# Kernel optimization log

Hardware: AMD Instinct MI355X
Metric: run time of the kernel (lower is better)

## Reference

```python
import jax, jax.numpy as jnp
import numpy as np

D_IN = 1024
D_OUT = 1024


def setup_inputs() -> dict:
    key = jax.random.key(0)
    ks = jax.random.split(key, 7)
    B, S = 4, 2048
    x = jax.random.normal(ks[0], (B, S, D_IN), dtype=jnp.float32)
    s = 1.0 / np.sqrt(D_IN)
    Wq = jax.random.uniform(ks[1], (D_IN, D_OUT), jnp.float32, -s, s)
    Wk = jax.random.uniform(ks[2], (D_IN, D_OUT), jnp.float32, -s, s)
    Wv = jax.random.uniform(ks[3], (D_IN, D_OUT), jnp.float32, -s, s)
    bq = jax.random.uniform(ks[4], (D_OUT,), jnp.float32, -s, s)
    bk = jax.random.uniform(ks[5], (D_OUT,), jnp.float32, -s, s)
    bv = jax.random.uniform(ks[6], (D_OUT,), jnp.float32, -s, s)
    return {"x": x, "Wq": Wq, "Wk": Wk, "Wv": Wv, "bq": bq, "bk": bk, "bv": bv}


def reference(x, Wq, Wk, Wv, bq, bk, bv):
    # x: [B, S, d_in]
    B, S, _ = x.shape
    q = x @ Wq + bq            # [B, S, d_out]
    k = x @ Wk + bk
    v = x @ Wv + bv
    scale = 1.0 / jnp.sqrt(jnp.asarray(q.shape[-1], q.dtype))
    scores = jnp.einsum('bqd,bkd->bqk', q, k)  # [B, S, S]
    causal = jnp.tril(jnp.ones((S, S), dtype=bool))
    scores = jnp.where(causal, scores, -jnp.inf)
    attn = jax.nn.softmax(scores * scale, axis=-1)
    return jnp.einsum('bqk,bkd->bqd', attn, v)
```

## Files before the change

kernel.cpp:

```cpp
#include <hip/hip_runtime.h>
#include <cstdint>

#define DEV __device__ __forceinline__

typedef __attribute__((ext_vector_type(4))) float f32x4;
typedef __attribute__((ext_vector_type(8))) short short8;
typedef __attribute__((ext_vector_type(4))) unsigned short u16x4;

constexpr int BS  = 4;
constexpr int SEQ = 2048;

DEV ushort f2b(float f){
  uint32_t u = __builtin_bit_cast(uint32_t, f);
  u += 0x7fffu + ((u >> 16) & 1u);
  return (ushort)(u >> 16);
}
DEV float b2f(ushort h){
  uint32_t u = (uint32_t)h << 16;
  return __builtin_bit_cast(float, u);
}

DEV void gload_lds16(const void* g, void* l){
  __builtin_amdgcn_global_load_lds(
      (const __attribute__((address_space(1))) unsigned int*)g,
      (__attribute__((address_space(3))) unsigned int*)l, 16, 0, 0);
}

#define BAR()    __builtin_amdgcn_s_barrier()
#define PRIO(x)  __builtin_amdgcn_s_setprio(x)
#define SCHEDB() __builtin_amdgcn_sched_barrier(0)
#define LGKM0()  asm volatile("s_waitcnt lgkmcnt(0)" ::: "memory")
#define LGKM8()  asm volatile("s_waitcnt lgkmcnt(8)" ::: "memory")
#define WAITV(n) asm volatile("s_waitcnt vmcnt(" #n ")" ::: "memory")

__global__ __launch_bounds__(256) void convert_f2b8(const float* __restrict__ src,
                                                    ushort* __restrict__ dst){
  long i = (long)blockIdx.x * 256 + threadIdx.x;
  const f32x4* s4 = (const f32x4*)src;
  f32x4 a = s4[i*2], b = s4[i*2+1];
  short8 o;
  o[0]=(short)f2b(a[0]); o[1]=(short)f2b(a[1]); o[2]=(short)f2b(a[2]); o[3]=(short)f2b(a[3]);
  o[4]=(short)f2b(b[0]); o[5]=(short)f2b(b[1]); o[6]=(short)f2b(b[2]); o[7]=(short)f2b(b[3]);
  ((short8*)dst)[i] = o;
}

__global__ __launch_bounds__(256) void transpose_f2b3(const float* __restrict__ w0,
                                                      const float* __restrict__ w1,
                                                      const float* __restrict__ w2,
                                                      ushort* __restrict__ dst){
  __shared__ float t[32][33];
  const int zz = blockIdx.z;
  const float* src = (zz == 0) ? w0 : (zz == 1) ? w1 : w2;
  ushort* d = dst + (long)zz * 1048576;
  int c0 = blockIdx.x * 32, r0 = blockIdx.y * 32;
  int tx = threadIdx.x, ty = threadIdx.y;
  #pragma unroll
  for (int k=0;k<4;k++) t[ty+k*8][tx] = src[(long)(r0+ty+k*8)*1024 + c0+tx];
  __syncthreads();
  #pragma unroll
  for (int k=0;k<4;k++) d[(long)(c0+ty+k*8)*1024 + r0+tx] = f2b(t[tx][ty+k*8]);
}

__global__ __launch_bounds__(256) void transpose_b2b(const ushort* __restrict__ src,
                                                     ushort* __restrict__ dst,
                                                     int R, int C){
  __shared__ ushort t[32][33];
  int c0 = blockIdx.x * 32, r0 = blockIdx.y * 32;
  int tx = threadIdx.x, ty = threadIdx.y;
  #pragma unroll
  for (int k=0;k<4;k++) t[ty+k*8][tx] = src[(long)(r0+ty+k*8)*C + c0+tx];
  __syncthreads();
  #pragma unroll
  for (int k=0;k<4;k++) dst[(long)(c0+ty+k*8)*R + r0+tx] = t[tx][ty+k*8];
}

struct GArgs {
  const ushort* A;  long lda; long aBS;
  const ushort* Bm; long ldb; long bBS;
  void* C;          long ldc; long cBS;
  const float* b0; const float* b1; const float* b2;
  int K;
};

__global__ __launch_bounds__(512, 2) void gemmA_qkv(GArgs g){
  extern __shared__ char sm[];
  const int tid = threadIdx.x;
  const int wid = tid >> 6, lane = tid & 63;
  const int wr = wid >> 2, wc = wid & 3;
  const int lr = lane & 15, lk = lane >> 4;
  const int f5 = ((lr >> 3) & 1) << 5;

  const int fid = blockIdx.x;
  const int xcd = fid & 7, j = fid >> 3;
  const int m0 = (xcd * 4 + (j & 3)) * 256;
  const int n0 = (j >> 2) * 192;

  const long lda2 = g.lda * 2, ldb2 = g.ldb * 2;
  const int skk = tid >> 8;
  const int srr = (tid >> 2) & 63;
  const int scc = tid & 3;
  const int scb = (scc * 16) ^ (((srr >> 3) & 1) << 5);
  const char* aU0 = (const char*)g.A  + (long)(m0       + srr)*lda2 + skk*64 + scb;
  const char* aU1 = (const char*)g.A  + (long)(m0 +  64 + srr)*lda2 + skk*64 + scb;
  const char* aU2 = (const char*)g.A  + (long)(m0 + 128 + srr)*lda2 + skk*64 + scb;
  const char* aU3 = (const char*)g.A  + (long)(m0 + 192 + srr)*lda2 + skk*64 + scb;
  const char* bU0 = (const char*)g.Bm + (long)(n0       + srr)*ldb2 + skk*64 + scb;
  const char* bU1 = (const char*)g.Bm + (long)(n0 +  64 + srr)*ldb2 + skk*64 + scb;
  const char* bU2 = (const char*)g.Bm + (long)(n0 + 128 + srr)*ldb2 + skk*64 + scb;
  const int dst = tid * 16;

#define STA(u, cb, k0) gload_lds16(aU##u + (k0)*2, sm + (cb)*57344 + u*8192 + dst)
#define STB(u, cb, k0) gload_lds16(bU##u + (k0)*2, sm + (cb)*57344 + 32768 + u*8192 + dst)

  int aoff[8], boff[3];
  #pragma unroll
  for (int mm=0;mm<8;mm++)
    aoff[mm] = wr*16384 + (mm>>2)*8192 + (mm&3)*1024 + lr*64 + ((lk*16) ^ f5);
  #pragma unroll
  for (int nn=0;nn<3;nn++){
    int br = wc*48 + nn*16 + lr;
    boff[nn] = 32768 + (br>>6)*8192 + (br&63)*64 + ((lk*16) ^ f5);
  }

  f32x4 acc[8][3];
  #pragma unroll
  for (int m=0;m<8;m++)
    #pragma unroll
    for (int n=0;n<3;n++) acc[m][n] = f32x4{0.f,0.f,0.f,0.f};

  const int NT = g.K >> 6;
  STA(0,0,0); STA(1,0,0); STA(2,0,0); STA(3,0,0);
  STB(0,0,0); STB(1,0,0); STB(2,0,0);
  STB(0,1,64); STB(1,1,64); STB(2,1,64);
  WAITV(3); BAR();

  short8 bf[3][2], af[2][2];
#define READ_AF(MB) \
    af[0][0] = *(const short8*)(base + aoff[MB  ]);        \
    af[0][1] = *(const short8*)(base + aoff[MB  ] + 4096); \
    af[1][0] = *(const short8*)(base + aoff[MB+1]);        \
    af[1][1] = *(const short8*)(base + aoff[MB+1] + 4096);
#define MFMA6(MB) \
    PRIO(1); \
    _Pragma("unroll") \
    for (int kk=0;kk<2;kk++) \
      _Pragma("unroll") \
      for (int mm=0;mm<2;mm++) \
        _Pragma("unroll") \
        for (int nn=0;nn<3;nn++) \
          acc[MB+mm][nn] = __builtin_amdgcn_mfma_f32_16x16x32_bf16(af[mm][kk], bf[nn][kk], acc[MB+mm][nn], 0,0,0); \
    PRIO(0);

  for (int t = 0; t < NT; ++t){
    const int c = t & 1;
    const char* base = sm + c*57344;
    const int kA = ((t+1) < NT ? (t+1) : NT-1) << 6;
    const int kB = ((t+2) < NT ? (t+2) : NT-1) << 6;
    STA(0, c^1, kA); STA(1, c^1, kA);
    #pragma unroll
    for (int nn=0;nn<3;nn++){
      bf[nn][0] = *(const short8*)(base + boff[nn]);
      bf[nn][1] = *(const short8*)(base + boff[nn] + 4096);
    }
    READ_AF(0);
    LGKM0(); SCHEDB();
    MFMA6(0);
    BAR();
    STA(2, c^1, kA); STA(3, c^1, kA);
    READ_AF(2);
    LGKM0(); SCHEDB();
    MFMA6(2);
    BAR();
    STB(0, c, kB); STB(1, c, kB);
    READ_AF(4);
    LGKM0(); SCHEDB();
    MFMA6(4);
    BAR();
    STB(2, c, kB);
    READ_AF(6);
    LGKM0(); SCHEDB();
    MFMA6(6);
    WAITV(3);
    BAR();
  }
  WAITV(0);
#undef STA
#undef STB
#undef READ_AF
#undef MFMA6

  #pragma unroll
  for (int nn=0;nn<3;nn++){
    int col  = n0 + wc*48 + nn*16 + lr;
    int sel  = col >> 10;
    int colq = col & 1023;
    const float* bp = (sel == 0) ? g.b0 : (sel == 1) ? g.b1 : g.b2;
    float bv = bp[colq];
    ushort* Cq = (ushort*)g.C + (long)sel * 8388608;
    #pragma unroll
    for (int mm=0;mm<8;mm++){
      int row0 = m0 + wr*128 + mm*16 + lk*4;
      #pragma unroll
      for (int i=0;i<4;i++)
        Cq[(long)(row0+i)*1024 + colq] = f2b(acc[mm][nn][i] + bv);
    }
  }
}

__global__ __launch_bounds__(512, 2) void scores8p(GArgs g){
  extern __shared__ char sm[];
  const int m0 = blockIdx.x * 256, n0 = blockIdx.y * 256;
  const int z  = blockIdx.z;
  if (n0 > m0) return;
  const int tid = threadIdx.x;
  const int wid = tid >> 6, lane = tid & 63;
  const int wr = wid >> 2, wc = wid & 3;
  const int lr = lane & 15, lk = lane >> 4;

  const char* Ab = (const char*)(g.A  + (long)z * g.aBS);
  const char* Bb = (const char*)(g.Bm + (long)z * g.bBS);
  const long lda2 = g.lda * 2, ldb2 = g.ldb * 2;
  const int srow = tid >> 2;
  const int scol = ((tid & 3) << 4) ^ (((tid >> 5) & 1) << 5);
  const char* sA = Ab + (long)(m0 + srow) * lda2 + scol;
  const char* sB = Bb + (long)(n0 + srow) * ldb2 + scol;
  const int dst16 = tid << 4;

  auto STAGE = [&](int tt, int which){
    const char* s = (which < 2)
        ? sA + (long)(which & 1) * 128 * lda2 + (long)tt * 128
        : sB + (long)(which & 1) * 128 * ldb2 + (long)tt * 128;
    char* d = sm + (tt & 1) * 65536 + which * 16384 + dst16;
    gload_lds16(s,      d);
    gload_lds16(s + 64, d + 8192);
  };

  int aoff[8], boff[4];
  #pragma unroll
  for (int mm = 0; mm < 8; mm++){
    int r = mm * 16 + lr;
    aoff[mm] = wr * 16384 + r * 64 + ((lk * 16) ^ (((r >> 3) & 1) << 5));
  }
  #pragma unroll
  for (int nn = 0; nn < 4; nn++){
    int rb = wc * 64 + nn * 16 + lr;
    boff[nn] = 32768 + (rb >> 7) * 16384 + (rb & 127) * 64
             + ((lk * 16) ^ (((rb >> 3) & 1) << 5));
  }

  f32x4 acc[8][4];
  #pragma unroll
  for (int m = 0; m < 8; m++)
    #pragma unroll
    for (int n = 0; n < 4; n++) acc[m][n] = f32x4{0.f,0.f,0.f,0.f};

  const int NT = g.K >> 6;
  STAGE(0,2); STAGE(0,3); STAGE(0,0); STAGE(0,1);
  STAGE(1,2); STAGE(1,3);
  WAITV(4); BAR();

  short8 af[2][2], bf[4][2];
#define READ_A(MB) \
    af[0][0] = *(const short8*)(base + aoff[MB]);            \
    af[0][1] = *(const short8*)(base + aoff[MB] + 8192);     \
    af[1][0] = *(const short8*)(base + aoff[MB+1]);          \
    af[1][1] = *(const short8*)(base + aoff[MB+1] + 8192);
#define MFMA16(MB) \
    PRIO(1); \
    _Pragma("unroll") \
    for (int kk = 0; kk < 2; kk++) \
      _Pragma("unroll") \
      for (int mm = 0; mm < 2; mm++) \
        _Pragma("unroll") \
        for (int nn = 0; nn < 4; nn++) \
          acc[MB+mm][nn] = __builtin_amdgcn_mfma_f32_16x16x32_bf16(af[mm][kk], bf[nn][kk], acc[MB+mm][nn], 0,0,0); \
    PRIO(0);

  for (int t = 0; t < NT; ++t){
    const char* base = sm + (t & 1) * 65536;
    if (t + 1 < NT) STAGE(t+1, 0);
    #pragma unroll
    for (int nn = 0; nn < 4; nn++){
      bf[nn][0] = *(const short8*)(base + boff[nn]);
      bf[nn][1] = *(const short8*)(base + boff[nn] + 8192);
    }
    READ_A(0);
    LGKM8();
    SCHEDB(); BAR(); LGKM0(); SCHEDB();
    MFMA16(0);
    SCHEDB(); BAR();
    if (t + 1 < NT) STAGE(t+1, 1);
    READ_A(2);
    SCHEDB(); BAR(); LGKM0(); SCHEDB();
    MFMA16(2);
    SCHEDB(); BAR();
    if (t + 2 < NT) STAGE(t+2, 2);
    READ_A(4);
    SCHEDB(); BAR(); LGKM0(); SCHEDB();
    MFMA16(4);
    SCHEDB(); BAR();
    if (t + 2 < NT) STAGE(t+2, 3);
    READ_A(6);
    SCHEDB(); BAR(); LGKM0(); SCHEDB();
    MFMA16(6);
    WAITV(4);
    SCHEDB(); BAR();
  }
#undef READ_A
#undef MFMA16

  const float scale = 0.03125f;
  ushort* Cs = (ushort*)g.C + (long)z * g.cBS;
  #pragma unroll
  for (int mm = 0; mm < 8; mm++){
    int row0 = m0 + wr*128 + mm*16 + lk*4;
    #pragma unroll
    for (int nn = 0; nn < 4; nn++){
      int col = n0 + wc*64 + nn*16 + lr;
      #pragma unroll
      for (int i = 0; i < 4; i++){
        int row = row0 + i;
        float e = (col <= row) ? __expf(acc[mm][nn][i] * scale) : 0.0f;
        Cs[(long)row*g.ldc + col] = f2b(e);
      }
    }
  }
}

__global__ __launch_bounds__(256) void rowsum_inv(const ushort* __restrict__ P,
                                                  float* __restrict__ inv){
  int row = blockIdx.x & (SEQ-1);
  int b   = blockIdx.x >> 11;
  const short8* pr = (const short8*)(P + ((long)b*SEQ + row)*(long)SEQ);
  int tid = threadIdx.x;
  int lane = tid & 63, wid = tid >> 6;
  float s = 0.f;
  if (tid*8 <= row){
    short8 v = pr[tid];
    #pragma unroll
    for (int j=0;j<8;j++) s += b2f((ushort)v[j]);
  }
  #pragma unroll
  for (int off=1; off<64; off<<=1) s += __shfl_xor(s, off);
  __shared__ float rb[4];
  if (lane == 0) rb[wid] = s;
  __syncthreads();
  if (tid == 0){
    float tot = (rb[0]+rb[1]) + (rb[2]+rb[3]);
    inv[(long)b*SEQ + row] = 1.0f / tot;
  }
}

__global__ __launch_bounds__(512, 2) void gemmPV(GArgs g){
  extern __shared__ char sm[];
  const int m0 = blockIdx.x * 128, n0 = blockIdx.y * 256;
  const int z  = blockIdx.z;
  const int tid = threadIdx.x;
  const int wid = tid >> 6, lane = tid & 63;
  const int wr = wid >> 2, wc = wid & 3;
  const int lr = lane & 15, lk = lane >> 4;
  const int f5 = ((lr >> 3) & 1) << 5;

  const char* Ab = (const char*)(g.A  + (long)z * g.aBS);
  const char* Bb = (const char*)(g.Bm + (long)z * g.bBS);
  const long lda2 = g.lda * 2, ldb2 = g.ldb * 2;
  const int sr  = tid >> 2;
  const int scb = ((lane & 3) << 4) ^ (((sr >> 3) & 1) << 5);
  const char* ar0 = Ab + (long)(m0 + sr)*lda2 + scb;
  const char* br0 = Bb + (long)(n0 + sr      )*ldb2 + scb;
  const char* br1 = Bb + (long)(n0 + 128 + sr)*ldb2 + scb;
  const int dwo = wid << 10;

  auto ST = [&](const char* row, int c, int off, int k0){
    const char* p = row + k0*2;
    char* d = sm + c*49152 + off + dwo;
    gload_lds16(p,      d);
    gload_lds16(p + 64, d + 8192);
  };

  const int aoffs = (wr*64 + lr)*64 + ((lk*16) ^ f5);
  const int boffs = 16384 + (wc>>1)*16384 + ((wc&1)*64 + lr)*64 + ((lk*16) ^ f5);

  f32x4 acc[4][4];
  #pragma unroll
  for (int m=0;m<4;m++)
    #pragma unroll
    for (int n=0;n<4;n++) acc[m][n] = f32x4{0.f,0.f,0.f,0.f};

  const int Keff = m0 + 128;
  const int NT = Keff >> 6;
  ST(ar0, 0, 0, 0);
  ST(br0, 0, 16384, 0); ST(br1, 0, 32768, 0);
  ST(br0, 1, 16384, 64); ST(br1, 1, 32768, 64);
  WAITV(4); BAR();

  for (int t = 0; t < NT; ++t){
    const int c = t & 1;
    const char* base = sm + c*49152;
    const int kA = ((t+1) < NT ? (t+1) : NT-1) << 6;
    const int kB = ((t+2) < NT ? (t+2) : NT-1) << 6;
    short8 bf[4][2], af[2][2];
    ST(ar0, c^1, 0, kA);
    #pragma unroll
    for (int n=0;n<4;n++)
      #pragma unroll
      for (int kk=0;kk<2;kk++)
        bf[n][kk] = *(const short8*)(base + boffs + kk*8192 + n*1024);
    #pragma unroll
    for (int mm=0;mm<2;mm++)
      #pragma unroll
      for (int kk=0;kk<2;kk++)
        af[mm][kk] = *(const short8*)(base + aoffs + kk*8192 + mm*1024);
    LGKM0(); SCHEDB();
    PRIO(1);
    #pragma unroll
    for (int kk=0;kk<2;kk++)
      #pragma unroll
      for (int mm=0;mm<2;mm++)
        #pragma unroll
        for (int n=0;n<4;n++)
          acc[mm][n] = __builtin_amdgcn_mfma_f32_16x16x32_bf16(af[mm][kk], bf[n][kk], acc[mm][n], 0,0,0);
    PRIO(0);
    BAR();
    ST(br0, c, 16384, kB); ST(br1, c, 32768, kB);
    #pragma unroll
    for (int mm=0;mm<2;mm++)
      #pragma unroll
      for (int kk=0;kk<2;kk++)
        af[mm][kk] = *(const short8*)(base + aoffs + kk*8192 + (2+mm)*1024);
    LGKM0(); SCHEDB();
    PRIO(1);
    #pragma unroll
    for (int kk=0;kk<2;kk++)
      #pragma unroll
      for (int mm=0;mm<2;mm++)
        #pragma unroll
        for (int n=0;n<4;n++)
          acc[2+mm][n] = __builtin_amdgcn_mfma_f32_16x16x32_bf16(af[mm][kk], bf[n][kk], acc[2+mm][n], 0,0,0);
    PRIO(0);
    WAITV(4);
    BAR();
  }
  WAITV(0);

  const float* invp = g.b0 + (long)z * SEQ;
  long cz = (long)z * g.cBS;
  #pragma unroll
  for (int m=0;m<4;m++){
    int row0 = m0 + wr*64 + m*16 + lk*4;
    #pragma unroll
    for (int n=0;n<4;n++){
      int col = n0 + wc*64 + n*16 + lr;
      #pragma unroll
      for (int i=0;i<4;i++)
        ((float*)g.C)[cz + (long)(row0+i)*g.ldc + col] = acc[m][n][i] * invp[row0+i];
    }
  }
}

extern "C" void kernel_launch(void* const* d_in, const int* in_sizes, int n_in,
                              void* d_out, int out_size, void* d_ws, size_t ws_size,
                              hipStream_t stream){
  const float* x  = (const float*)d_in[0];
  const float* Wq = (const float*)d_in[1];
  const float* Wk = (const float*)d_in[2];
  const float* Wv = (const float*)d_in[3];
  const float* bq = (const float*)d_in[4];
  const float* bk = (const float*)d_in[5];
  const float* bv = (const float*)d_in[6];
  float* out = (float*)d_out;

  const long XB = 0;
  const long WT = 16777216;
  const long QB = 23068672;
  const long VT = 73400320;
  const long PU = 90177536;
  const long IV = 123731968;
  const long NEED = 123764736;
  if ((long)ws_size < NEED) return;

  char* ws = (char*)d_ws;
  ushort* xb = (ushort*)(ws + XB);
  ushort* wt = (ushort*)(ws + WT);
  ushort* qb = (ushort*)(ws + QB);
  ushort* kb = qb + 8388608;
  ushort* vb = qb + 16777216;
  ushort* vt = (ushort*)(ws + VT);
  ushort* pu = (ushort*)(ws + PU);
  float*  iv = (float* )(ws + IV);

  hipFuncSetAttribute(reinterpret_cast<const void*>(&gemmA_qkv),
                      hipFuncAttributeMaxDynamicSharedMemorySize, 114688);
  hipFuncSetAttribute(reinterpret_cast<const void*>(&scores8p),
                      hipFuncAttributeMaxDynamicSharedMemorySize, 131072);
  hipFuncSetAttribute(reinterpret_cast<const void*>(&gemmPV),
                      hipFuncAttributeMaxDynamicSharedMemorySize, 98304);

  dim3 tb(32, 8);

  convert_f2b8<<<4096, 256, 0, stream>>>(x, xb);
  transpose_f2b3<<<dim3(32,32,3), tb, 0, stream>>>(Wq, Wk, Wv, wt);

  GArgs pa{};
  pa.A = xb; pa.lda = 1024; pa.aBS = 0;
  pa.Bm = wt; pa.ldb = 1024; pa.bBS = 0;
  pa.C = (void*)qb; pa.ldc = 1024; pa.cBS = 0;
  pa.b0 = bq; pa.b1 = bk; pa.b2 = bv;
  pa.K = 1024;
  gemmA_qkv<<<512, 512, 114688, stream>>>(pa);

  transpose_b2b<<<dim3(32,256), tb, 0, stream>>>(vb, vt, 8192, 1024);

  GArgs sa{};
  sa.A = qb;  sa.lda = 1024; sa.aBS = (long)SEQ*1024;
  sa.Bm = kb; sa.ldb = 1024; sa.bBS = (long)SEQ*1024;
  sa.C = (void*)pu; sa.ldc = SEQ; sa.cBS = (long)SEQ*SEQ;
  sa.b0 = nullptr; sa.b1 = nullptr; sa.b2 = nullptr;
  sa.K = 1024;
  scores8p<<<dim3(8,8,4), 512, 131072, stream>>>(sa);

  rowsum_inv<<<BS*SEQ, 256, 0, stream>>>(pu, iv);

  GArgs va{};
  va.A = pu;  va.lda = SEQ;  va.aBS = (long)SEQ*SEQ;
  va.Bm = vt; va.ldb = 8192; va.bBS = SEQ;
  va.C = (void*)out; va.ldc = 1024; va.cBS = (long)SEQ*1024;
  va.b0 = iv; va.b1 = nullptr; va.b2 = nullptr;
  va.K = SEQ;
  gemmPV<<<dim3(16,4,4), 512, 98304, stream>>>(va);
}
```

Before: 169.5 us.

## Replace scores and PV GEMMs with simpler 128x128 tiles and paired causal PV blocks

Replaces the hand-scheduled 256x256 scores kernel and the 128x256 PV kernel with simpler 128x128-tile, 256-thread kernels using static LDS and a plain double-buffered K=32 loop. The PV kernel pairs causal row tile px with tile 15-px in one block, so every block does about the same amount of work. The goal is better load balance and occupancy on the triangular workload. The cost is losing the fine-grained barrier/priority interleaving, the LDS swizzle and the larger tiles, so LDS bank conflicts and per-tile overhead may rise.

```diff
diff --git a/kernel.cpp b/kernel.cpp
--- a/kernel.cpp
+++ b/kernel.cpp
@@ -30,7 +30,6 @@
 #define PRIO(x)  __builtin_amdgcn_s_setprio(x)
 #define SCHEDB() __builtin_amdgcn_sched_barrier(0)
 #define LGKM0()  asm volatile("s_waitcnt lgkmcnt(0)" ::: "memory")
-#define LGKM8()  asm volatile("s_waitcnt lgkmcnt(8)" ::: "memory")
 #define WAITV(n) asm volatile("s_waitcnt vmcnt(" #n ")" ::: "memory")
 
 __global__ __launch_bounds__(256) void convert_f2b8(const float* __restrict__ src,
@@ -207,120 +206,83 @@
   }
 }
 
-__global__ __launch_bounds__(512, 2) void scores8p(GArgs g){
-  extern __shared__ char sm[];
-  const int m0 = blockIdx.x * 256, n0 = blockIdx.y * 256;
-  const int z  = blockIdx.z;
+__global__ __launch_bounds__(256) void scoresE(GArgs g){
+  __shared__ ushort aL[2][128*32];
+  __shared__ ushort bL[2][128*32];
+  int m0 = blockIdx.x * 128, n0 = blockIdx.y * 128;
+  int z  = blockIdx.z;
   if (n0 > m0) return;
-  const int tid = threadIdx.x;
-  const int wid = tid >> 6, lane = tid & 63;
-  const int wr = wid >> 2, wc = wid & 3;
-  const int lr = lane & 15, lk = lane >> 4;
-
   const char* Ab = (const char*)(g.A  + (long)z * g.aBS);
   const char* Bb = (const char*)(g.Bm + (long)z * g.bBS);
-  const long lda2 = g.lda * 2, ldb2 = g.ldb * 2;
-  const int srow = tid >> 2;
-  const int scol = ((tid & 3) << 4) ^ (((tid >> 5) & 1) << 5);
-  const char* sA = Ab + (long)(m0 + srow) * lda2 + scol;
-  const char* sB = Bb + (long)(n0 + srow) * ldb2 + scol;
-  const int dst16 = tid << 4;
-
-  auto STAGE = [&](int tt, int which){
-    const char* s = (which < 2)
-        ? sA + (long)(which & 1) * 128 * lda2 + (long)tt * 128
-        : sB + (long)(which & 1) * 128 * ldb2 + (long)tt * 128;
-    char* d = sm + (tt & 1) * 65536 + which * 16384 + dst16;
-    gload_lds16(s,      d);
-    gload_lds16(s + 64, d + 8192);
+  int tid = threadIdx.x;
+  int wid = tid >> 6, lane = tid & 63;
+  int wr = wid >> 1, wc = wid & 1;
+  int lr = lane & 15, lk = lane >> 4;
+
+  int ob0 = (0*4 + wid) * 1024;
+  int ob1 = (1*4 + wid) * 1024;
+  int o0  = ob0 + (lane << 4);
+  int o1  = ob1 + (lane << 4);
+  int r0_ = o0 >> 6, cb0 = o0 & 63;
+  int r1_ = o1 >> 6, cb1 = o1 & 63;
+
+  auto stage = [&](int buf, int k0){
+    gload_lds16(Ab + ((long)(m0+r0_)*g.lda + k0)*2 + cb0, (char*)aL[buf] + ob0);
+    gload_lds16(Bb + ((long)(n0+r0_)*g.ldb + k0)*2 + cb0, (char*)bL[buf] + ob0);
+    gload_lds16(Ab + ((long)(m0+r1_)*g.lda + k0)*2 + cb1, (char*)aL[buf] + ob1);
+    gload_lds16(Bb + ((long)(n0+r1_)*g.ldb + k0)*2 + cb1, (char*)bL[buf] + ob1);
   };
 
-  int aoff[8], boff[4];
-  #pragma unroll
-  for (int mm = 0; mm < 8; mm++){
-    int r = mm * 16 + lr;
-    aoff[mm] = wr * 16384 + r * 64 + ((lk * 16) ^ (((r >> 3) & 1) << 5));
-  }
-  #pragma unroll
-  for (int nn = 0; nn < 4; nn++){
-    int rb = wc * 64 + nn * 16 + lr;
-    boff[nn] = 32768 + (rb >> 7) * 16384 + (rb & 127) * 64
-             + ((lk * 16) ^ (((rb >> 3) & 1) << 5));
-  }
-
-  f32x4 acc[8][4];
-  #pragma unroll
-  for (int m = 0; m < 8; m++)
-    #pragma unroll
-    for (int n = 0; n < 4; n++) acc[m][n] = f32x4{0.f,0.f,0.f,0.f};
-
-  const int NT = g.K >> 6;
-  STAGE(0,2); STAGE(0,3); STAGE(0,0); STAGE(0,1);
-  STAGE(1,2); STAGE(1,3);
-  WAITV(4); BAR();
-
-  short8 af[2][2], bf[4][2];
-#define READ_A(MB) \
-    af[0][0] = *(const short8*)(base + aoff[MB]);            \
-    af[0][1] = *(const short8*)(base + aoff[MB] + 8192);     \
-    af[1][0] = *(const short8*)(base + aoff[MB+1]);          \
-    af[1][1] = *(const short8*)(base + aoff[MB+1] + 8192);
-#define MFMA16(MB) \
-    PRIO(1); \
-    _Pragma("unroll") \
-    for (int kk = 0; kk < 2; kk++) \
-      _Pragma("unroll") \
-      for (int mm = 0; mm < 2; mm++) \
-        _Pragma("unroll") \
-        for (int nn = 0; nn < 4; nn++) \
-          acc[MB+mm][nn] = __builtin_amdgcn_mfma_f32_16x16x32_bf16(af[mm][kk], bf[nn][kk], acc[MB+mm][nn], 0,0,0); \
-    PRIO(0);
-
-  for (int t = 0; t < NT; ++t){
-    const char* base = sm + (t & 1) * 65536;
-    if (t + 1 < NT) STAGE(t+1, 0);
-    #pragma unroll
-    for (int nn = 0; nn < 4; nn++){
-      bf[nn][0] = *(const short8*)(base + boff[nn]);
-      bf[nn][1] = *(const short8*)(base + boff[nn] + 8192);
-    }
-    READ_A(0);
-    LGKM8();
-    SCHEDB(); BAR(); LGKM0(); SCHEDB();
-    MFMA16(0);
-    SCHEDB(); BAR();
-    if (t + 1 < NT) STAGE(t+1, 1);
-    READ_A(2);
-    SCHEDB(); BAR(); LGKM0(); SCHEDB();
-    MFMA16(2);
-    SCHEDB(); BAR();
-    if (t + 2 < NT) STAGE(t+2, 2);
-    READ_A(4);
-    SCHEDB(); BAR(); LGKM0(); SCHEDB();
-    MFMA16(4);
-    SCHEDB(); BAR();
-    if (t + 2 < NT) STAGE(t+2, 3);
-    READ_A(6);
-    SCHEDB(); BAR(); LGKM0(); SCHEDB();
-    MFMA16(6);
-    WAITV(4);
-    SCHEDB(); BAR();
-  }
-#undef READ_A
-#undef MFMA16
+  f32x4 acc[4][4];
+  #pragma unroll
+  for (int m=0;m<4;m++)
+    #pragma unroll
+    for (int n=0;n<4;n++) acc[m][n] = f32x4{0.f,0.f,0.f,0.f};
+
+  int nt = g.K >> 5;
+  stage(0, 0);
+  __syncthreads();
+  int cur = 0;
+  for (int t = 0; t < nt-1; ++t){
+    stage(cur ^ 1, (t+1) << 5);
+    short8 af[4], bf4[4];
+    #pragma unroll
+    for (int m=0;m<4;m++) af[m]  = *(const short8*)&aL[cur][(wr*64 + m*16 + lr)*32 + lk*8];
+    #pragma unroll
+    for (int n=0;n<4;n++) bf4[n] = *(const short8*)&bL[cur][(wc*64 + n*16 + lr)*32 + lk*8];
+    #pragma unroll
+    for (int m=0;m<4;m++)
+      #pragma unroll
+      for (int n=0;n<4;n++)
+        acc[m][n] = __builtin_amdgcn_mfma_f32_16x16x32_bf16(af[m], bf4[n], acc[m][n], 0, 0, 0);
+    __syncthreads();
+    cur ^= 1;
+  }
+  {
+    short8 af[4], bf4[4];
+    #pragma unroll
+    for (int m=0;m<4;m++) af[m]  = *(const short8*)&aL[cur][(wr*64 + m*16 + lr)*32 + lk*8];
+    #pragma unroll
+    for (int n=0;n<4;n++) bf4[n] = *(const short8*)&bL[cur][(wc*64 + n*16 + lr)*32 + lk*8];
+    #pragma unroll
+    for (int m=0;m<4;m++)
+      #pragma unroll
+      for (int n=0;n<4;n++)
+        acc[m][n] = __builtin_amdgcn_mfma_f32_16x16x32_bf16(af[m], bf4[n], acc[m][n], 0, 0, 0);
+  }
 
   const float scale = 0.03125f;
   ushort* Cs = (ushort*)g.C + (long)z * g.cBS;
   #pragma unroll
-  for (int mm = 0; mm < 8; mm++){
-    int row0 = m0 + wr*128 + mm*16 + lk*4;
-    #pragma unroll
-    for (int nn = 0; nn < 4; nn++){
-      int col = n0 + wc*64 + nn*16 + lr;
-      #pragma unroll
-      for (int i = 0; i < 4; i++){
+  for (int m=0;m<4;m++){
+    int row0 = m0 + wr*64 + m*16 + lk*4;
+    #pragma unroll
+    for (int n=0;n<4;n++){
+      int col = n0 + wc*64 + n*16 + lr;
+      #pragma unroll
+      for (int i=0;i<4;i++){
         int row = row0 + i;
-        float e = (col <= row) ? __expf(acc[mm][nn][i] * scale) : 0.0f;
+        float e = (col <= row) ? __expf(acc[m][n][i] * scale) : 0.0f;
         Cs[(long)row*g.ldc + col] = f2b(e);
       }
     }
@@ -351,110 +313,91 @@
   }
 }
 
-__global__ __launch_bounds__(512, 2) void gemmPV(GArgs g){
-  extern __shared__ char sm[];
-  const int m0 = blockIdx.x * 128, n0 = blockIdx.y * 256;
+__global__ __launch_bounds__(256) void pvPair(GArgs g){
+  __shared__ ushort aL[2][128*32];
+  __shared__ ushort bL[2][128*32];
+  const int px = blockIdx.x;
+  const int n0 = blockIdx.y * 128;
   const int z  = blockIdx.z;
-  const int tid = threadIdx.x;
-  const int wid = tid >> 6, lane = tid & 63;
-  const int wr = wid >> 2, wc = wid & 3;
-  const int lr = lane & 15, lk = lane >> 4;
-  const int f5 = ((lr >> 3) & 1) << 5;
-
   const char* Ab = (const char*)(g.A  + (long)z * g.aBS);
   const char* Bb = (const char*)(g.Bm + (long)z * g.bBS);
-  const long lda2 = g.lda * 2, ldb2 = g.ldb * 2;
-  const int sr  = tid >> 2;
-  const int scb = ((lane & 3) << 4) ^ (((sr >> 3) & 1) << 5);
-  const char* ar0 = Ab + (long)(m0 + sr)*lda2 + scb;
-  const char* br0 = Bb + (long)(n0 + sr      )*ldb2 + scb;
-  const char* br1 = Bb + (long)(n0 + 128 + sr)*ldb2 + scb;
-  const int dwo = wid << 10;
-
-  auto ST = [&](const char* row, int c, int off, int k0){
-    const char* p = row + k0*2;
-    char* d = sm + c*49152 + off + dwo;
-    gload_lds16(p,      d);
-    gload_lds16(p + 64, d + 8192);
-  };
-
-  const int aoffs = (wr*64 + lr)*64 + ((lk*16) ^ f5);
-  const int boffs = 16384 + (wc>>1)*16384 + ((wc&1)*64 + lr)*64 + ((lk*16) ^ f5);
-
-  f32x4 acc[4][4];
-  #pragma unroll
-  for (int m=0;m<4;m++)
-    #pragma unroll
-    for (int n=0;n<4;n++) acc[m][n] = f32x4{0.f,0.f,0.f,0.f};
-
-  const int Keff = m0 + 128;
-  const int NT = Keff >> 6;
-  ST(ar0, 0, 0, 0);
-  ST(br0, 0, 16384, 0); ST(br1, 0, 32768, 0);
-  ST(br0, 1, 16384, 64); ST(br1, 1, 32768, 64);
-  WAITV(4); BAR();
-
-  for (int t = 0; t < NT; ++t){
-    const int c = t & 1;
-    const char* base = sm + c*49152;
-    const int kA = ((t+1) < NT ? (t+1) : NT-1) << 6;
-    const int kB = ((t+2) < NT ? (t+2) : NT-1) << 6;
-    short8 bf[4][2], af[2][2];
-    ST(ar0, c^1, 0, kA);
-    #pragma unroll
-    for (int n=0;n<4;n++)
-      #pragma unroll
-      for (int kk=0;kk<2;kk++)
-        bf[n][kk] = *(const short8*)(base + boffs + kk*8192 + n*1024);
-    #pragma unroll
-    for (int mm=0;mm<2;mm++)
-      #pragma unroll
-      for (int kk=0;kk<2;kk++)
-        af[mm][kk] = *(const short8*)(base + aoffs + kk*8192 + mm*1024);
-    LGKM0(); SCHEDB();
-    PRIO(1);
-    #pragma unroll
-    for (int kk=0;kk<2;kk++)
-      #pragma unroll
-      for (int mm=0;mm<2;mm++)
+  const float* invp = g.b0 + (long)z * SEQ;
+  float* Co = (float*)g.C + (long)z * g.cBS;
+  int tid = threadIdx.x;
+  int wid = tid >> 6, lane = tid & 63;
+  int wr = wid >> 1, wc = wid & 1;
+  int lr = lane & 15, lk = lane >> 4;
+
+  int ob0 = (0*4 + wid) * 1024;
+  int ob1 = (1*4 + wid) * 1024;
+  int o0  = ob0 + (lane << 4);
+  int o1  = ob1 + (lane << 4);
+  int r0_ = o0 >> 6, cb0 = o0 & 63;
+  int r1_ = o1 >> 6, cb1 = o1 & 63;
+
+  #pragma unroll
+  for (int half = 0; half < 2; ++half){
+    const int mt = half ? (15 - px) : px;
+    const int m0 = mt * 128;
+    const int Keff = m0 + 128;
+
+    auto stage = [&](int buf, int k0){
+      gload_lds16(Ab + ((long)(m0+r0_)*g.lda + k0)*2 + cb0, (char*)aL[buf] + ob0);
+      gload_lds16(Bb + ((long)(n0+r0_)*g.ldb + k0)*2 + cb0, (char*)bL[buf] + ob0);
+      gload_lds16(Ab + ((long)(m0+r1_)*g.lda + k0)*2 + cb1, (char*)aL[buf] + ob1);
+      gload_lds16(Bb + ((long)(n0+r1_)*g.ldb + k0)*2 + cb1, (char*)bL[buf] + ob1);
+    };
+
+    f32x4 acc[4][4];
+    #pragma unroll
+    for (int m=0;m<4;m++)
+      #pragma unroll
+      for (int n=0;n<4;n++) acc[m][n] = f32x4{0.f,0.f,0.f,0.f};
+
+    int nt = Keff >> 5;
+    stage(0, 0);
+    __syncthreads();
+    int cur = 0;
+    for (int t = 0; t < nt-1; ++t){
+      stage(cur ^ 1, (t+1) << 5);
+      short8 af[4], bf4[4];
+      #pragma unroll
+      for (int m=0;m<4;m++) af[m]  = *(const short8*)&aL[cur][(wr*64 + m*16 + lr)*32 + lk*8];
+      #pragma unroll
+      for (int n=0;n<4;n++) bf4[n] = *(const short8*)&bL[cur][(wc*64 + n*16 + lr)*32 + lk*8];
+      #pragma unroll
+      for (int m=0;m<4;m++)
         #pragma unroll
         for (int n=0;n<4;n++)
-          acc[mm][n] = __builtin_amdgcn_mfma_f32_16x16x32_bf16(af[mm][kk], bf[n][kk], acc[mm][n], 0,0,0);
-    PRIO(0);
-    BAR();
-    ST(br0, c, 16384, kB); ST(br1, c, 32768, kB);
-    #pragma unroll
-    for (int mm=0;mm<2;mm++)
-      #pragma unroll
-      for (int kk=0;kk<2;kk++)
-        af[mm][kk] = *(const short8*)(base + aoffs + kk*8192 + (2+mm)*1024);
-    LGKM0(); SCHEDB();
-    PRIO(1);
-    #pragma unroll
-    for (int kk=0;kk<2;kk++)
-      #pragma unroll
-      for (int mm=0;mm<2;mm++)
+          acc[m][n] = __builtin_amdgcn_mfma_f32_16x16x32_bf16(af[m], bf4[n], acc[m][n], 0, 0, 0);
+      __syncthreads();
+      cur ^= 1;
+    }
+    {
+      short8 af[4], bf4[4];
+      #pragma unroll
+      for (int m=0;m<4;m++) af[m]  = *(const short8*)&aL[cur][(wr*64 + m*16 + lr)*32 + lk*8];
+      #pragma unroll
+      for (int n=0;n<4;n++) bf4[n] = *(const short8*)&bL[cur][(wc*64 + n*16 + lr)*32 + lk*8];
+      #pragma unroll
+      for (int m=0;m<4;m++)
         #pragma unroll
         for (int n=0;n<4;n++)
-          acc[2+mm][n] = __builtin_amdgcn_mfma_f32_16x16x32_bf16(af[mm][kk], bf[n][kk], acc[2+mm][n], 0,0,0);
-    PRIO(0);
-    WAITV(4);
-    BAR();
-  }
-  WAITV(0);
-
-  const float* invp = g.b0 + (long)z * SEQ;
-  long cz = (long)z * g.cBS;
-  #pragma unroll
-  for (int m=0;m<4;m++){
-    int row0 = m0 + wr*64 + m*16 + lk*4;
-    #pragma unroll
-    for (int n=0;n<4;n++){
-      int col = n0 + wc*64 + n*16 + lr;
-      #pragma unroll
-      for (int i=0;i<4;i++)
-        ((float*)g.C)[cz + (long)(row0+i)*g.ldc + col] = acc[m][n][i] * invp[row0+i];
-    }
+          acc[m][n] = __builtin_amdgcn_mfma_f32_16x16x32_bf16(af[m], bf4[n], acc[m][n], 0, 0, 0);
+    }
+
+    #pragma unroll
+    for (int m=0;m<4;m++){
+      int row0 = m0 + wr*64 + m*16 + lk*4;
+      #pragma unroll
+      for (int n=0;n<4;n++){
+        int col = n0 + wc*64 + n*16 + lr;
+        #pragma unroll
+        for (int i=0;i<4;i++)
+          Co[(long)(row0+i)*g.ldc + col] = acc[m][n][i] * invp[row0+i];
+      }
+    }
+    __syncthreads();
   }
 }
 
@@ -491,10 +434,6 @@
 
   hipFuncSetAttribute(reinterpret_cast<const void*>(&gemmA_qkv),
                       hipFuncAttributeMaxDynamicSharedMemorySize, 114688);
-  hipFuncSetAttribute(reinterpret_cast<const void*>(&scores8p),
-                      hipFuncAttributeMaxDynamicSharedMemorySize, 131072);
-  hipFuncSetAttribute(reinterpret_cast<const void*>(&gemmPV),
-                      hipFuncAttributeMaxDynamicSharedMemorySize, 98304);
 
   dim3 tb(32, 8);
 
@@ -517,7 +456,7 @@
   sa.C = (void*)pu; sa.ldc = SEQ; sa.cBS = (long)SEQ*SEQ;
   sa.b0 = nullptr; sa.b1 = nullptr; sa.b2 = nullptr;
   sa.K = 1024;
-  scores8p<<<dim3(8,8,4), 512, 131072, stream>>>(sa);
+  scoresE<<<dim3(16,16,BS), 256, 0, stream>>>(sa);
 
   rowsum_inv<<<BS*SEQ, 256, 0, stream>>>(pu, iv);
 
@@ -527,5 +466,5 @@
   va.C = (void*)out; va.ldc = 1024; va.cBS = (long)SEQ*1024;
   va.b0 = iv; va.b1 = nullptr; va.b2 = nullptr;
   va.K = SEQ;
-  gemmPV<<<dim3(16,4,4), 512, 98304, stream>>>(va);
-}
+  pvPair<<<dim3(8,8,BS), 256, 0, stream>>>(va);
+}
```

Result: slower. 217.6 us (+28.4%).

## Retile causal scores GEMM to 256x128 tiles with compact triangular grid

Applied to the files above, without the earlier changes.

Replaces the 256x256-tile scores kernel, which launched a full 8x8 grid and early-exited the upper-triangle blocks, with a 256x128 tile kernel. A 1-D grid of 288 blocks is mapped only onto the needed lower-triangular tiles. The smaller tile cuts LDS use from 128KB to 96KB, raises the block count for better CU load balance, and reworks the staging and barrier schedule with simpler waits. In exchange each block does less data reuse per loaded A tile, so A is reloaded more often.

```diff
diff --git a/kernel.cpp b/kernel.cpp
--- a/kernel.cpp
+++ b/kernel.cpp
@@ -30,7 +30,6 @@
 #define PRIO(x)  __builtin_amdgcn_s_setprio(x)
 #define SCHEDB() __builtin_amdgcn_sched_barrier(0)
 #define LGKM0()  asm volatile("s_waitcnt lgkmcnt(0)" ::: "memory")
-#define LGKM8()  asm volatile("s_waitcnt lgkmcnt(8)" ::: "memory")
 #define WAITV(n) asm volatile("s_waitcnt vmcnt(" #n ")" ::: "memory")
 
 __global__ __launch_bounds__(256) void convert_f2b8(const float* __restrict__ src,
@@ -207,118 +206,128 @@
   }
 }
 
-__global__ __launch_bounds__(512, 2) void scores8p(GArgs g){
+__global__ __launch_bounds__(512, 2) void scoresX(GArgs g){
   extern __shared__ char sm[];
-  const int m0 = blockIdx.x * 256, n0 = blockIdx.y * 256;
-  const int z  = blockIdx.z;
-  if (n0 > m0) return;
   const int tid = threadIdx.x;
   const int wid = tid >> 6, lane = tid & 63;
   const int wr = wid >> 2, wc = wid & 3;
   const int lr = lane & 15, lk = lane >> 4;
+  const int f5 = ((lr >> 3) & 1) << 5;
+
+  const int bid = blockIdx.x;
+  const int z   = bid / 72;
+  const int idp = bid - z * 72;
+  int m = 0;
+  #pragma unroll
+  for (int mm = 1; mm < 8; ++mm) if (idp >= mm*(mm+1)) m = mm;
+  const int n  = idp - m*(m+1);
+  const int m0 = m * 256, n0 = n * 128;
 
   const char* Ab = (const char*)(g.A  + (long)z * g.aBS);
   const char* Bb = (const char*)(g.Bm + (long)z * g.bBS);
   const long lda2 = g.lda * 2, ldb2 = g.ldb * 2;
-  const int srow = tid >> 2;
-  const int scol = ((tid & 3) << 4) ^ (((tid >> 5) & 1) << 5);
-  const char* sA = Ab + (long)(m0 + srow) * lda2 + scol;
-  const char* sB = Bb + (long)(n0 + srow) * ldb2 + scol;
-  const int dst16 = tid << 4;
-
-  auto STAGE = [&](int tt, int which){
-    const char* s = (which < 2)
-        ? sA + (long)(which & 1) * 128 * lda2 + (long)tt * 128
-        : sB + (long)(which & 1) * 128 * ldb2 + (long)tt * 128;
-    char* d = sm + (tt & 1) * 65536 + which * 16384 + dst16;
-    gload_lds16(s,      d);
-    gload_lds16(s + 64, d + 8192);
-  };
-
-  int aoff[8], boff[4];
-  #pragma unroll
-  for (int mm = 0; mm < 8; mm++){
-    int r = mm * 16 + lr;
-    aoff[mm] = wr * 16384 + r * 64 + ((lk * 16) ^ (((r >> 3) & 1) << 5));
-  }
-  #pragma unroll
-  for (int nn = 0; nn < 4; nn++){
-    int rb = wc * 64 + nn * 16 + lr;
-    boff[nn] = 32768 + (rb >> 7) * 16384 + (rb & 127) * 64
-             + ((lk * 16) ^ (((rb >> 3) & 1) << 5));
-  }
-
-  f32x4 acc[8][4];
-  #pragma unroll
-  for (int m = 0; m < 8; m++)
-    #pragma unroll
-    for (int n = 0; n < 4; n++) acc[m][n] = f32x4{0.f,0.f,0.f,0.f};
+  const int skk = tid >> 8;
+  const int srr = (tid >> 2) & 63;
+  const int scc = tid & 3;
+  const int scb = (scc * 16) ^ (((srr >> 3) & 1) << 5);
+  const char* aU0 = Ab + (long)(m0       + srr)*lda2 + skk*64 + scb;
+  const char* aU1 = Ab + (long)(m0 +  64 + srr)*lda2 + skk*64 + scb;
+  const char* aU2 = Ab + (long)(m0 + 128 + srr)*lda2 + skk*64 + scb;
+  const char* aU3 = Ab + (long)(m0 + 192 + srr)*lda2 + skk*64 + scb;
+  const char* bU0 = Bb + (long)(n0       + srr)*ldb2 + skk*64 + scb;
+  const char* bU1 = Bb + (long)(n0 +  64 + srr)*ldb2 + skk*64 + scb;
+  const int dst = tid * 16;
+
+#define STA(u, cb, k0) gload_lds16(aU##u + (k0)*2, sm + (cb)*49152 + u*8192 + dst)
+#define STB(u, cb, k0) gload_lds16(bU##u + (k0)*2, sm + (cb)*49152 + 32768 + u*8192 + dst)
+
+  int aoff[8], boff[2];
+  #pragma unroll
+  for (int mm=0;mm<8;mm++)
+    aoff[mm] = wr*16384 + (mm>>2)*8192 + (mm&3)*1024 + lr*64 + ((lk*16) ^ f5);
+  #pragma unroll
+  for (int nn=0;nn<2;nn++){
+    int br = wc*32 + nn*16 + lr;
+    boff[nn] = 32768 + (br>>6)*8192 + (br&63)*64 + ((lk*16) ^ f5);
+  }
+
+  f32x4 acc[8][2];
+  #pragma unroll
+  for (int m2=0;m2<8;m2++)
+    #pragma unroll
+    for (int n2=0;n2<2;n2++) acc[m2][n2] = f32x4{0.f,0.f,0.f,0.f};
 
   const int NT = g.K >> 6;
-  STAGE(0,2); STAGE(0,3); STAGE(0,0); STAGE(0,1);
-  STAGE(1,2); STAGE(1,3);
-  WAITV(4); BAR();
-
-  short8 af[2][2], bf[4][2];
-#define READ_A(MB) \
-    af[0][0] = *(const short8*)(base + aoff[MB]);            \
-    af[0][1] = *(const short8*)(base + aoff[MB] + 8192);     \
-    af[1][0] = *(const short8*)(base + aoff[MB+1]);          \
-    af[1][1] = *(const short8*)(base + aoff[MB+1] + 8192);
-#define MFMA16(MB) \
+  STA(0,0,0); STA(1,0,0); STA(2,0,0); STA(3,0,0);
+  STB(0,0,0); STB(1,0,0);
+  STB(0,1,64); STB(1,1,64);
+  WAITV(2); BAR();
+
+  short8 bf[2][2], af[2][2];
+#define READ_AF(MB) \
+    af[0][0] = *(const short8*)(base + aoff[MB  ]);        \
+    af[0][1] = *(const short8*)(base + aoff[MB  ] + 4096); \
+    af[1][0] = *(const short8*)(base + aoff[MB+1]);        \
+    af[1][1] = *(const short8*)(base + aoff[MB+1] + 4096);
+#define MFMA4(MB) \
     PRIO(1); \
     _Pragma("unroll") \
-    for (int kk = 0; kk < 2; kk++) \
+    for (int kk=0;kk<2;kk++) \
       _Pragma("unroll") \
-      for (int mm = 0; mm < 2; mm++) \
+      for (int mm=0;mm<2;mm++) \
         _Pragma("unroll") \
-        for (int nn = 0; nn < 4; nn++) \
+        for (int nn=0;nn<2;nn++) \
           acc[MB+mm][nn] = __builtin_amdgcn_mfma_f32_16x16x32_bf16(af[mm][kk], bf[nn][kk], acc[MB+mm][nn], 0,0,0); \
     PRIO(0);
 
   for (int t = 0; t < NT; ++t){
-    const char* base = sm + (t & 1) * 65536;
-    if (t + 1 < NT) STAGE(t+1, 0);
-    #pragma unroll
-    for (int nn = 0; nn < 4; nn++){
+    const int c = t & 1;
+    const char* base = sm + c*49152;
+    const int kA = ((t+1) < NT ? (t+1) : NT-1) << 6;
+    const int kB = ((t+2) < NT ? (t+2) : NT-1) << 6;
+    STA(0, c^1, kA); STA(1, c^1, kA);
+    #pragma unroll
+    for (int nn=0;nn<2;nn++){
       bf[nn][0] = *(const short8*)(base + boff[nn]);
-      bf[nn][1] = *(const short8*)(base + boff[nn] + 8192);
+      bf[nn][1] = *(const short8*)(base + boff[nn] + 4096);
     }
-    READ_A(0);
-    LGKM8();
-    SCHEDB(); BAR(); LGKM0(); SCHEDB();
-    MFMA16(0);
-    SCHEDB(); BAR();
-    if (t + 1 < NT) STAGE(t+1, 1);
-    READ_A(2);
-    SCHEDB(); BAR(); LGKM0(); SCHEDB();
-    MFMA16(2);
-    SCHEDB(); BAR();
-    if (t + 2 < NT) STAGE(t+2, 2);
-    READ_A(4);
-    SCHEDB(); BAR(); LGKM0(); SCHEDB();
-    MFMA16(4);
-    SCHEDB(); BAR();
-    if (t + 2 < NT) STAGE(t+2, 3);
-    READ_A(6);
-    SCHEDB(); BAR(); LGKM0(); SCHEDB();
-    MFMA16(6);
-    WAITV(4);
-    SCHEDB(); BAR();
-  }
-#undef READ_A
-#undef MFMA16
+    READ_AF(0);
+    LGKM0(); SCHEDB();
+    MFMA4(0);
+    BAR();
+    STA(2, c^1, kA); STA(3, c^1, kA);
+    READ_AF(2);
+    LGKM0(); SCHEDB();
+    MFMA4(2);
+    BAR();
+    STB(0, c, kB);
+    READ_AF(4);
+    LGKM0(); SCHEDB();
+    MFMA4(4);
+    BAR();
+    STB(1, c, kB);
+    READ_AF(6);
+    LGKM0(); SCHEDB();
+    MFMA4(6);
+    WAITV(2);
+    BAR();
+  }
+  WAITV(0);
+#undef STA
+#undef STB
+#undef READ_AF
+#undef MFMA4
 
   const float scale = 0.03125f;
   ushort* Cs = (ushort*)g.C + (long)z * g.cBS;
   #pragma unroll
-  for (int mm = 0; mm < 8; mm++){
-    int row0 = m0 + wr*128 + mm*16 + lk*4;
-    #pragma unroll
-    for (int nn = 0; nn < 4; nn++){
-      int col = n0 + wc*64 + nn*16 + lr;
-      #pragma unroll
-      for (int i = 0; i < 4; i++){
+  for (int nn=0;nn<2;nn++){
+    int col = n0 + wc*32 + nn*16 + lr;
+    #pragma unroll
+    for (int mm=0;mm<8;mm++){
+      int row0 = m0 + wr*128 + mm*16 + lk*4;
+      #pragma unroll
+      for (int i=0;i<4;i++){
         int row = row0 + i;
         float e = (col <= row) ? __expf(acc[mm][nn][i] * scale) : 0.0f;
         Cs[(long)row*g.ldc + col] = f2b(e);
@@ -491,8 +500,8 @@
 
   hipFuncSetAttribute(reinterpret_cast<const void*>(&gemmA_qkv),
                       hipFuncAttributeMaxDynamicSharedMemorySize, 114688);
-  hipFuncSetAttribute(reinterpret_cast<const void*>(&scores8p),
-                      hipFuncAttributeMaxDynamicSharedMemorySize, 131072);
+  hipFuncSetAttribute(reinterpret_cast<const void*>(&scoresX),
+                      hipFuncAttributeMaxDynamicSharedMemorySize, 98304);
   hipFuncSetAttribute(reinterpret_cast<const void*>(&gemmPV),
                       hipFuncAttributeMaxDynamicSharedMemorySize, 98304);
 
@@ -517,7 +526,7 @@
   sa.C = (void*)pu; sa.ldc = SEQ; sa.cBS = (long)SEQ*SEQ;
   sa.b0 = nullptr; sa.b1 = nullptr; sa.b2 = nullptr;
   sa.K = 1024;
-  scores8p<<<dim3(8,8,4), 512, 131072, stream>>>(sa);
+  scoresX<<<288, 512, 98304, stream>>>(sa);
 
   rowsum_inv<<<BS*SEQ, 256, 0, stream>>>(pu, iv);
 
```

Result: slower. 175.8 us (+3.7%).

## Fuse V transpose into QKV epilogue and row sums into scores kernel

Applied to the files above, without the earlier changes.

The QKV GEMM epilogue now writes V directly in transposed layout (4-element vector stores along the sequence), which removes the separate transpose_b2b kernel. The scores kernel accumulates per-row sums of the exponentials with lane shuffles and atomicAdd into a buffer zeroed by a memset, which removes the rowsum_inv pass over the full score matrix. PV then divides by the sums directly. This trades two kernels and an extra read of P and V for atomics and a memset, and the transposed V stores are less coalesced.

```diff
diff --git a/kernel.cpp b/kernel.cpp
--- a/kernel.cpp
+++ b/kernel.cpp
@@ -14,10 +14,6 @@
   uint32_t u = __builtin_bit_cast(uint32_t, f);
   u += 0x7fffu + ((u >> 16) & 1u);
   return (ushort)(u >> 16);
-}
-DEV float b2f(ushort h){
-  uint32_t u = (uint32_t)h << 16;
-  return __builtin_bit_cast(float, u);
 }
 
 DEV void gload_lds16(const void* g, void* l){
@@ -61,23 +57,12 @@
   for (int k=0;k<4;k++) d[(long)(c0+ty+k*8)*1024 + r0+tx] = f2b(t[tx][ty+k*8]);
 }
 
-__global__ __launch_bounds__(256) void transpose_b2b(const ushort* __restrict__ src,
-                                                     ushort* __restrict__ dst,
-                                                     int R, int C){
-  __shared__ ushort t[32][33];
-  int c0 = blockIdx.x * 32, r0 = blockIdx.y * 32;
-  int tx = threadIdx.x, ty = threadIdx.y;
-  #pragma unroll
-  for (int k=0;k<4;k++) t[ty+k*8][tx] = src[(long)(r0+ty+k*8)*C + c0+tx];
-  __syncthreads();
-  #pragma unroll
-  for (int k=0;k<4;k++) dst[(long)(c0+ty+k*8)*R + r0+tx] = t[tx][ty+k*8];
-}
-
 struct GArgs {
   const ushort* A;  long lda; long aBS;
   const ushort* Bm; long ldb; long bBS;
   void* C;          long ldc; long cBS;
+  void* C2;
+  float* sums;
   const float* b0; const float* b1; const float* b2;
   int K;
 };
@@ -196,13 +181,25 @@
     int colq = col & 1023;
     const float* bp = (sel == 0) ? g.b0 : (sel == 1) ? g.b1 : g.b2;
     float bv = bp[colq];
-    ushort* Cq = (ushort*)g.C + (long)sel * 8388608;
-    #pragma unroll
-    for (int mm=0;mm<8;mm++){
-      int row0 = m0 + wr*128 + mm*16 + lk*4;
-      #pragma unroll
-      for (int i=0;i<4;i++)
-        Cq[(long)(row0+i)*1024 + colq] = f2b(acc[mm][nn][i] + bv);
+    if (sel == 2){
+      ushort* Vt = (ushort*)g.C2;
+      #pragma unroll
+      for (int mm=0;mm<8;mm++){
+        int row0 = m0 + wr*128 + mm*16 + lk*4;
+        u16x4 o;
+        #pragma unroll
+        for (int i=0;i<4;i++) o[i] = f2b(acc[mm][nn][i] + bv);
+        *(u16x4*)(Vt + (long)colq*8192 + row0) = o;
+      }
+    } else {
+      ushort* Cq = (ushort*)g.C + (long)sel * 8388608;
+      #pragma unroll
+      for (int mm=0;mm<8;mm++){
+        int row0 = m0 + wr*128 + mm*16 + lk*4;
+        #pragma unroll
+        for (int i=0;i<4;i++)
+          Cq[(long)(row0+i)*1024 + colq] = f2b(acc[mm][nn][i] + bv);
+      }
     }
   }
 }
@@ -311,43 +308,25 @@
 
   const float scale = 0.03125f;
   ushort* Cs = (ushort*)g.C + (long)z * g.cBS;
+  float* sums = g.sums + (long)z * SEQ;
   #pragma unroll
   for (int mm = 0; mm < 8; mm++){
     int row0 = m0 + wr*128 + mm*16 + lk*4;
     #pragma unroll
-    for (int nn = 0; nn < 4; nn++){
-      int col = n0 + wc*64 + nn*16 + lr;
-      #pragma unroll
-      for (int i = 0; i < 4; i++){
-        int row = row0 + i;
+    for (int i = 0; i < 4; i++){
+      int row = row0 + i;
+      float s = 0.f;
+      #pragma unroll
+      for (int nn = 0; nn < 4; nn++){
+        int col = n0 + wc*64 + nn*16 + lr;
         float e = (col <= row) ? __expf(acc[mm][nn][i] * scale) : 0.0f;
         Cs[(long)row*g.ldc + col] = f2b(e);
+        s += e;
       }
+      s += __shfl_xor(s, 1); s += __shfl_xor(s, 2);
+      s += __shfl_xor(s, 4); s += __shfl_xor(s, 8);
+      if (lr == 0) atomicAdd(&sums[row], s);
     }
-  }
-}
-
-__global__ __launch_bounds__(256) void rowsum_inv(const ushort* __restrict__ P,
-                                                  float* __restrict__ inv){
-  int row = blockIdx.x & (SEQ-1);
-  int b   = blockIdx.x >> 11;
-  const short8* pr = (const short8*)(P + ((long)b*SEQ + row)*(long)SEQ);
-  int tid = threadIdx.x;
-  int lane = tid & 63, wid = tid >> 6;
-  float s = 0.f;
-  if (tid*8 <= row){
-    short8 v = pr[tid];
-    #pragma unroll
-    for (int j=0;j<8;j++) s += b2f((ushort)v[j]);
-  }
-  #pragma unroll
-  for (int off=1; off<64; off<<=1) s += __shfl_xor(s, off);
-  __shared__ float rb[4];
-  if (lane == 0) rb[wid] = s;
-  __syncthreads();
-  if (tid == 0){
-    float tot = (rb[0]+rb[1]) + (rb[2]+rb[3]);
-    inv[(long)b*SEQ + row] = 1.0f / tot;
   }
 }
 
@@ -443,17 +422,20 @@
   }
   WAITV(0);
 
-  const float* invp = g.b0 + (long)z * SEQ;
+  const float* sums = g.sums + (long)z * SEQ;
   long cz = (long)z * g.cBS;
   #pragma unroll
   for (int m=0;m<4;m++){
     int row0 = m0 + wr*64 + m*16 + lk*4;
+    float iv4[4];
+    #pragma unroll
+    for (int i=0;i<4;i++) iv4[i] = 1.0f / sums[row0+i];
     #pragma unroll
     for (int n=0;n<4;n++){
       int col = n0 + wc*64 + n*16 + lr;
       #pragma unroll
       for (int i=0;i<4;i++)
-        ((float*)g.C)[cz + (long)(row0+i)*g.ldc + col] = acc[m][n][i] * invp[row0+i];
+        ((float*)g.C)[cz + (long)(row0+i)*g.ldc + col] = acc[m][n][i] * iv4[i];
     }
   }
 }
@@ -484,7 +466,6 @@
   ushort* wt = (ushort*)(ws + WT);
   ushort* qb = (ushort*)(ws + QB);
   ushort* kb = qb + 8388608;
-  ushort* vb = qb + 16777216;
   ushort* vt = (ushort*)(ws + VT);
   ushort* pu = (ushort*)(ws + PU);
   float*  iv = (float* )(ws + IV);
@@ -498,6 +479,7 @@
 
   dim3 tb(32, 8);
 
+  hipMemsetAsync(iv, 0, BS*SEQ*sizeof(float), stream);
   convert_f2b8<<<4096, 256, 0, stream>>>(x, xb);
   transpose_f2b3<<<dim3(32,32,3), tb, 0, stream>>>(Wq, Wk, Wv, wt);
 
@@ -505,27 +487,26 @@
   pa.A = xb; pa.lda = 1024; pa.aBS = 0;
   pa.Bm = wt; pa.ldb = 1024; pa.bBS = 0;
   pa.C = (void*)qb; pa.ldc = 1024; pa.cBS = 0;
+  pa.C2 = (void*)vt; pa.sums = nullptr;
   pa.b0 = bq; pa.b1 = bk; pa.b2 = bv;
   pa.K = 1024;
   gemmA_qkv<<<512, 512, 114688, stream>>>(pa);
-
-  transpose_b2b<<<dim3(32,256), tb, 0, stream>>>(vb, vt, 8192, 1024);
 
   GArgs sa{};
   sa.A = qb;  sa.lda = 1024; sa.aBS = (long)SEQ*1024;
   sa.Bm = kb; sa.ldb = 1024; sa.bBS = (long)SEQ*1024;
   sa.C = (void*)pu; sa.ldc = SEQ; sa.cBS = (long)SEQ*SEQ;
+  sa.C2 = nullptr; sa.sums = iv;
   sa.b0 = nullptr; sa.b1 = nullptr; sa.b2 = nullptr;
   sa.K = 1024;
   scores8p<<<dim3(8,8,4), 512, 131072, stream>>>(sa);
-
-  rowsum_inv<<<BS*SEQ, 256, 0, stream>>>(pu, iv);
 
   GArgs va{};
   va.A = pu;  va.lda = SEQ;  va.aBS = (long)SEQ*SEQ;
   va.Bm = vt; va.ldb = 8192; va.bBS = SEQ;
   va.C = (void*)out; va.ldc = 1024; va.cBS = (long)SEQ*1024;
-  va.b0 = iv; va.b1 = nullptr; va.b2 = nullptr;
+  va.C2 = nullptr; va.sums = iv;
+  va.b0 = nullptr; va.b1 = nullptr; va.b2 = nullptr;
   va.K = SEQ;
   gemmPV<<<dim3(16,4,4), 512, 98304, stream>>>(va);
 }
```

Result: faster. 160.4 us (-5.4%).
